# Performance work log

Measured on AMD Instinct MI355X. Metric: run time of the kernel, lower is better.

Reference implementation:

```python
import jax, jax.numpy as jnp
import numpy as np
from jax import lax

DIM = 2048
N_HEADS = 16
N_KV = 4
HEAD_DIM = DIM // N_HEADS  # 128
ROPE_BASE = 10000.0
SEQ = 4096
BSZ = 1


def bitlinear(x, W):
    # per-row abs-mean scale (detached), ternary round/clamp, straight-through blend
    s = lax.stop_gradient(jnp.clip(jnp.mean(jnp.abs(W), axis=1, keepdims=True), 1e-5, None))
    wt = jnp.clip(jnp.round(W / s), -1.0, 1.0)
    w = lax.stop_gradient(wt - W) + W  # straight-through
    return x @ (w * s).T


def rms_norm(x):
    eps = jnp.finfo(x.dtype).eps
    return x * lax.rsqrt(jnp.mean(x * x, axis=-1, keepdims=True) + eps)


def rope(x, cos, sin):
    half = x.shape[-1] // 2
    x1, x2 = x[..., :half], x[..., half:]
    return jnp.concatenate((x1 * cos + x2 * sin, -x1 * sin + x2 * cos), axis=-1)


def setup_inputs() -> dict:
    key = jax.random.key(0)
    ks = jax.random.split(key, 6)
    kv_dim = N_KV * HEAD_DIM
    return {
        "x": jax.random.normal(ks[0], (BSZ, SEQ, DIM), dtype=jnp.float32),
        "wq": jax.random.normal(ks[1], (DIM, DIM), dtype=jnp.float32) * 0.02,
        "wk": jax.random.normal(ks[2], (kv_dim, DIM), dtype=jnp.float32) * 0.02,
        "wv": jax.random.normal(ks[3], (kv_dim, DIM), dtype=jnp.float32) * 0.02,
        "wp": jax.random.normal(ks[4], (DIM, DIM), dtype=jnp.float32) * 0.02,
        "q_gain": jnp.ones((N_HEADS,), dtype=jnp.float32),
    }


def reference(x, wq, wk, wv, wp, q_gain):
    b, s, d = x.shape
    q = bitlinear(x, wq).reshape(b, s, N_HEADS, HEAD_DIM).transpose(0, 2, 1, 3)  # bhsd
    k = bitlinear(x, wk).reshape(b, s, N_KV, HEAD_DIM).transpose(0, 2, 1, 3)
    v = bitlinear(x, wv).reshape(b, s, N_KV, HEAD_DIM).transpose(0, 2, 1, 3)

    q = rms_norm(q)
    k = rms_norm(k)

    inv_freq = 1.0 / ROPE_BASE ** (jnp.arange(0, HEAD_DIM, 2, dtype=jnp.float32) / HEAD_DIM)
    t = jnp.arange(s, dtype=jnp.float32)
    freqs = jnp.outer(t, inv_freq)  # [s, hd/2]
    cos = jnp.cos(freqs)[None, None].astype(q.dtype)
    sin = jnp.sin(freqs)[None, None].astype(q.dtype)
    q = rope(q, cos, sin)
    k = rope(k, cos, sin)

    q = q * q_gain.astype(q.dtype)[None, :, None, None]

    groups = N_HEADS // N_KV
    k = jnp.repeat(k, groups, axis=1)  # GQA expand to [b, H, s, hd]
    v = jnp.repeat(v, groups, axis=1)

    scale = 1.0 / np.sqrt(HEAD_DIM)
    scores = jnp.einsum("bhqd,bhkd->bhqk", q, k) * scale
    causal = jnp.tril(jnp.ones((s, s), dtype=bool))
    scores = jnp.where(causal[None, None], scores, jnp.finfo(scores.dtype).min)
    attn = jax.nn.softmax(scores, axis=-1)
    y = jnp.einsum("bhqk,bhkd->bhqd", attn, v)

    y = y.transpose(0, 2, 1, 3).reshape(b, s, d)
    return bitlinear(y, wp)
```

## Files before the change

kernel.cpp:

```cpp
#include <hip/hip_runtime.h>
#include <math.h>

typedef unsigned short u16;
typedef short s16x8 __attribute__((ext_vector_type(8)));
typedef float f32x4 __attribute__((ext_vector_type(4)));
typedef u16 u16x4 __attribute__((ext_vector_type(4)));

static constexpr size_t OFF_XB   = 0;
static constexpr size_t OFF_WQKV = 16777216;
static constexpr size_t OFF_WP   = 29360128;
static constexpr size_t OFF_QKV  = 37748736;
static constexpr size_t OFF_PART = 37748736 + 16777216;
static constexpr size_t OFF_KH   = 88080384;
static constexpr size_t OFF_VT   = 92274688;

__device__ __forceinline__ u16 f2bf(float f) {
  union { float f; unsigned u; } v; v.f = f;
  unsigned r = v.u + 0x7fffu + ((v.u >> 16) & 1u);
  return (u16)(r >> 16);
}

__device__ __forceinline__ void async16(const u16* g, u16* lds) {
  __builtin_amdgcn_global_load_lds(
      (const __attribute__((address_space(1))) void*)g,
      (__attribute__((address_space(3))) void*)lds, 16, 0, 0);
}

__global__ __launch_bounds__(256) void quant_rows(const float* __restrict__ W,
                                                  u16* __restrict__ out) {
  const int row = blockIdx.x, tid = threadIdx.x;
  const float* src = W + (size_t)row * 2048 + tid * 8;
  float4 a = *(const float4*)(src);
  float4 b = *(const float4*)(src + 4);
  float asum = fabsf(a.x)+fabsf(a.y)+fabsf(a.z)+fabsf(a.w)
             + fabsf(b.x)+fabsf(b.y)+fabsf(b.z)+fabsf(b.w);
  #pragma unroll
  for (int off = 1; off < 64; off <<= 1) asum += __shfl_xor(asum, off, 64);
  __shared__ float red[4];
  if ((tid & 63) == 0) red[tid >> 6] = asum;
  __syncthreads();
  float s = fmaxf((red[0]+red[1]+red[2]+red[3]) * (1.0f/2048.0f), 1e-5f);
  float v[8] = {a.x,a.y,a.z,a.w,b.x,b.y,b.z,b.w};
  u16* dst = out + (size_t)row * 2048 + tid * 8;
  #pragma unroll
  for (int i = 0; i < 8; i++) {
    float q = rintf(v[i] / s);
    q = fminf(fmaxf(q, -1.f), 1.f);
    dst[i] = f2bf(q * s);
  }
}

__global__ __launch_bounds__(256) void cvt_bf16(const float* __restrict__ in,
                                                u16* __restrict__ out) {
  size_t i = ((size_t)blockIdx.x * 256 + threadIdx.x) * 4;
  float4 v = *(const float4*)(in + i);
  u16x4 o;
  o.x = f2bf(v.x); o.y = f2bf(v.y); o.z = f2bf(v.z); o.w = f2bf(v.w);
  *(u16x4*)(out + i) = o;
}

__global__ __launch_bounds__(256) void gemm_bt(const u16* __restrict__ A,
                                               const u16* __restrict__ B,
                                               float* __restrict__ C,
                                               int M, int N, int K) {
  __shared__ u16 sA[128 * 32];
  __shared__ u16 sB[128 * 32];
  const int tid = threadIdx.x;
  const int lane = tid & 63;
  const int wid = tid >> 6;
  const int lr = lane & 15, lq = lane >> 4;
  const int wm = (wid >> 1) * 64, wn = (wid & 1) * 64;
  const size_t m0 = (size_t)blockIdx.y * 128, n0 = (size_t)blockIdx.x * 128;

  const int r0 = tid >> 2, c0 = (tid & 3) * 8;
  const u16* Ab0 = A + (m0 + r0) * (size_t)K + c0;
  const u16* Ab1 = A + (m0 + 64 + r0) * (size_t)K + c0;
  const u16* Bb0 = B + (n0 + r0) * (size_t)K + c0;
  const u16* Bb1 = B + (n0 + 64 + r0) * (size_t)K + c0;
  u16* sA0 = &sA[tid * 8];
  u16* sA1 = &sA[(256 + tid) * 8];
  u16* sB0 = &sB[tid * 8];
  u16* sB1 = &sB[(256 + tid) * 8];

  f32x4 acc[4][4] = {};

  for (int kt = 0; kt < K; kt += 32) {
    async16(Ab0 + kt, sA0);
    async16(Ab1 + kt, sA1);
    async16(Bb0 + kt, sB0);
    async16(Bb1 + kt, sB1);
    __syncthreads();
    s16x8 af[4], bf[4];
    #pragma unroll
    for (int mt = 0; mt < 4; mt++)
      af[mt] = *(const s16x8*)&sA[(wm + mt * 16 + lr) * 32 + lq * 8];
    #pragma unroll
    for (int nt = 0; nt < 4; nt++)
      bf[nt] = *(const s16x8*)&sB[(wn + nt * 16 + lr) * 32 + lq * 8];
    #pragma unroll
    for (int mt = 0; mt < 4; mt++)
      #pragma unroll
      for (int nt = 0; nt < 4; nt++)
        acc[mt][nt] = __builtin_amdgcn_mfma_f32_16x16x32_bf16(af[mt], bf[nt], acc[mt][nt], 0, 0, 0);
    __syncthreads();
  }
  #pragma unroll
  for (int mt = 0; mt < 4; mt++)
    #pragma unroll
    for (int nt = 0; nt < 4; nt++)
      #pragma unroll
      for (int r = 0; r < 4; r++) {
        size_t m = m0 + wm + mt * 16 + lq * 4 + r;
        size_t n = n0 + wn + nt * 16 + lr;
        C[m * (size_t)N + n] = acc[mt][nt][r];
      }
}

__global__ __launch_bounds__(256) void prep_qk(const float* __restrict__ qkv,
                                               const float* __restrict__ qgain,
                                               u16* __restrict__ Qh,
                                               u16* __restrict__ Kh) {
  const int s = blockIdx.y;
  const int j = blockIdx.x * 4 + (threadIdx.x >> 6);
  const int t = threadIdx.x & 63;
  const float* row = qkv + (size_t)s * 3072 + (size_t)j * 128;
  float x1 = row[t], x2 = row[t + 64];
  float ss = x1 * x1 + x2 * x2;
  #pragma unroll
  for (int off = 1; off < 64; off <<= 1) ss += __shfl_xor(ss, off, 64);
  float rn = rsqrtf(ss * (1.0f / 128.0f) + 1.1920929e-07f);
  float invf = exp2f(-(float)t * 0.20762050593048096f);
  float ang = (float)s * invf;
  float sn, c;
  sincosf(ang, &sn, &c);
  if (j < 16) {
    float g = qgain[j] * 0.12751738f;
    float q1 = x1 * rn, q2 = x2 * rn;
    float o1 = (q1 * c + q2 * sn) * g;
    float o2 = (-q1 * sn + q2 * c) * g;
    u16* dst = Qh + ((size_t)j * 4096 + s) * 128;
    dst[t] = f2bf(o1); dst[t + 64] = f2bf(o2);
  } else {
    float k1 = x1 * rn, k2 = x2 * rn;
    float o1 = k1 * c + k2 * sn;
    float o2 = -k1 * sn + k2 * c;
    u16* dst = Kh + ((size_t)(j - 16) * 4096 + s) * 128;
    dst[t] = f2bf(o1); dst[t + 64] = f2bf(o2);
  }
}

__global__ __launch_bounds__(256) void vtrans(const float* __restrict__ qkv,
                                              u16* __restrict__ Vtg) {
  __shared__ float tile[64][67];
  const int tid = threadIdx.x;
  const int s0 = blockIdx.y * 64;
  const int c0 = blockIdx.x * 64;
  #pragma unroll
  for (int it = 0; it < 4; it++) {
    int i = it * 256 + tid;
    int r = i >> 4, c = (i & 15) * 4;
    float4 v = *(const float4*)(qkv + (size_t)(s0 + r) * 3072 + 2560 + c0 + c);
    tile[r][c] = v.x; tile[r][c + 1] = v.y; tile[r][c + 2] = v.z; tile[r][c + 3] = v.w;
  }
  __syncthreads();
  #pragma unroll
  for (int it = 0; it < 2; it++) {
    int i = it * 256 + tid;
    int dl = i >> 3, sc = (i & 7) * 8;
    s16x8 ov;
    #pragma unroll
    for (int jj = 0; jj < 8; jj++) ov[jj] = (short)f2bf(tile[sc + jj][dl]);
    *(s16x8*)&Vtg[(size_t)(c0 + dl) * 4096 + s0 + sc] = ov;
  }
}

__global__ __launch_bounds__(256, 2) void attn(const u16* __restrict__ Q,
                                               const u16* __restrict__ Kh,
                                               const u16* __restrict__ Vt,
                                               u16* __restrict__ Y,
                                               float* __restrict__ Opart,
                                               float* __restrict__ MLpart) {
  const int tid = threadIdx.x, lane = tid & 63, wid = tid >> 6;
  const int lr = lane & 15, lq = lane >> 4;

  int rem = blockIdx.x, s = 32;
  for (;;) {
    int cnt = (s >= 17 ? 32 : 0) + (((s & 1) == 0) ? 16 : 0);
    if (rem < cnt) break;
    rem -= cnt; --s;
  }
  int qt, chunk, h, split;
  if (s >= 17 && rem < 32) { split = 1; qt = s - 1; chunk = rem >> 4; h = rem & 15; }
  else { split = 0; if (s >= 17) rem -= 32; qt = (s >> 1) - 1; chunk = 0; h = rem & 15; }
  const int t0 = split ? chunk * (qt + 1) : 0;
  const int t1 = split ? t0 + qt + 1 : 2 * qt + 2;
  const int kvh = h >> 2;
  const int qbase = qt * 128;

  __shared__ u16 sK[64][136];
  __shared__ u16 sVt[144][72];
  __shared__ u16 sP[4][32][72];

  for (int i = tid; i < 16 * 72; i += 256) {
    int r = i / 72, c = i - r * 72;
    sVt[128 + r][c] = (r == 0) ? (u16)0x3F80 : (u16)0;
  }

  s16x8 qf[2][4];
  #pragma unroll
  for (int f = 0; f < 2; f++) {
    const u16* qp = Q + ((size_t)h * 4096 + qbase + wid * 32 + f * 16 + lr) * 128 + lq * 8;
    #pragma unroll
    for (int kc = 0; kc < 4; kc++) qf[f][kc] = *(const s16x8*)(qp + kc * 32);
  }

  f32x4 oacc[2][9] = {};
  float mrow[2][4];
  #pragma unroll
  for (int f = 0; f < 2; f++)
    #pragma unroll
    for (int r = 0; r < 4; r++) mrow[f][r] = -1e30f;

  const u16* Kbase = Kh + (size_t)kvh * 4096 * 128;
  const u16* Vbase = Vt + (size_t)kvh * 128 * 4096;

  for (int t = t0; t < t1; ++t) {
    #pragma unroll
    for (int it = 0; it < 4; it++) {
      int idx = it * 256 + tid;
      int kr = idx >> 4, kc8 = (idx & 15) * 8;
      *(s16x8*)&sK[kr][kc8] = *(const s16x8*)(Kbase + (size_t)(t * 64 + kr) * 128 + kc8);
    }
    #pragma unroll
    for (int it = 0; it < 4; it++) {
      int idx = it * 256 + tid;
      int vd = idx >> 3, vc = (idx & 7) * 8;
      *(s16x8*)&sVt[vd][vc] = *(const s16x8*)(Vbase + (size_t)vd * 4096 + t * 64 + vc);
    }
    __syncthreads();

    f32x4 sacc[2][4] = {};
    #pragma unroll
    for (int nt = 0; nt < 4; nt++)
      #pragma unroll
      for (int kc = 0; kc < 4; kc++) {
        s16x8 kf = *(const s16x8*)&sK[nt * 16 + lr][kc * 32 + lq * 8];
        sacc[0][nt] = __builtin_amdgcn_mfma_f32_16x16x32_bf16(qf[0][kc], kf, sacc[0][nt], 0, 0, 0);
        sacc[1][nt] = __builtin_amdgcn_mfma_f32_16x16x32_bf16(qf[1][kc], kf, sacc[1][nt], 0, 0, 0);
      }

    if (t >= 2 * qt) {
      #pragma unroll
      for (int f = 0; f < 2; f++) {
        int qr0 = qbase + wid * 32 + f * 16 + lq * 4;
        #pragma unroll
        for (int nt = 0; nt < 4; nt++) {
          int col = t * 64 + nt * 16 + lr;
          #pragma unroll
          for (int r = 0; r < 4; r++)
            if (col > qr0 + r) sacc[f][nt][r] = -1e30f;
        }
      }
    }

    float mx[2][4];
    #pragma unroll
    for (int f = 0; f < 2; f++)
      #pragma unroll
      for (int r = 0; r < 4; r++)
        mx[f][r] = fmaxf(fmaxf(sacc[f][0][r], sacc[f][1][r]),
                         fmaxf(sacc[f][2][r], sacc[f][3][r]));
    #pragma unroll
    for (int off = 1; off < 16; off <<= 1)
      #pragma unroll
      for (int f = 0; f < 2; f++)
        #pragma unroll
        for (int r = 0; r < 4; r++) mx[f][r] = fmaxf(mx[f][r], __shfl_xor(mx[f][r], off, 64));

    bool grow = false;
    #pragma unroll
    for (int f = 0; f < 2; f++)
      #pragma unroll
      for (int r = 0; r < 4; r++) grow = grow || (mx[f][r] > mrow[f][r]);
    if (__any(grow)) {
      float al[2][4];
      #pragma unroll
      for (int f = 0; f < 2; f++)
        #pragma unroll
        for (int r = 0; r < 4; r++) {
          float mn = fmaxf(mrow[f][r], mx[f][r]);
          al[f][r] = exp2f(mrow[f][r] - mn);
          mrow[f][r] = mn;
        }
      #pragma unroll
      for (int f = 0; f < 2; f++)
        #pragma unroll
        for (int dt = 0; dt < 9; dt++)
          #pragma unroll
          for (int r = 0; r < 4; r++) oacc[f][dt][r] *= al[f][r];
    }

    #pragma unroll
    for (int f = 0; f < 2; f++)
      #pragma unroll
      for (int nt = 0; nt < 4; nt++)
        #pragma unroll
        for (int r = 0; r < 4; r++) {
          union { float fv; unsigned u; } pu;
          pu.fv = exp2f(sacc[f][nt][r] - mrow[f][r]);
          sP[wid][f * 16 + lq * 4 + r][nt * 16 + lr] = (u16)(pu.u >> 16);
        }

    #pragma unroll
    for (int kc = 0; kc < 2; kc++) {
      s16x8 pf0 = *(const s16x8*)&sP[wid][lr][kc * 32 + lq * 8];
      s16x8 pf1 = *(const s16x8*)&sP[wid][16 + lr][kc * 32 + lq * 8];
      #pragma unroll
      for (int dt = 0; dt < 9; dt++) {
        s16x8 vf = *(const s16x8*)&sVt[dt * 16 + lr][kc * 32 + lq * 8];
        oacc[0][dt] = __builtin_amdgcn_mfma_f32_16x16x32_bf16(pf0, vf, oacc[0][dt], 0, 0, 0);
        oacc[1][dt] = __builtin_amdgcn_mfma_f32_16x16x32_bf16(pf1, vf, oacc[1][dt], 0, 0, 0);
      }
    }
    __syncthreads();
  }

  if (split) {
    const int pidx = ((qt - 16) * 16 + h) * 2 + chunk;
    float* Op = Opart + (size_t)pidx * 16384;
    #pragma unroll
    for (int f = 0; f < 2; f++)
      #pragma unroll
      for (int dt = 0; dt < 8; dt++)
        #pragma unroll
        for (int r = 0; r < 4; r++)
          Op[(wid * 32 + f * 16 + lq * 4 + r) * 128 + dt * 16 + lr] = oacc[f][dt][r];
    if (lr == 0) {
      #pragma unroll
      for (int f = 0; f < 2; f++)
        #pragma unroll
        for (int r = 0; r < 4; r++) {
          int row = wid * 32 + f * 16 + lq * 4 + r;
          MLpart[(size_t)pidx * 256 + row * 2]     = mrow[f][r];
          MLpart[(size_t)pidx * 256 + row * 2 + 1] = oacc[f][8][r];
        }
    }
  } else {
    #pragma unroll
    for (int f = 0; f < 2; f++) {
      float linv[4];
      #pragma unroll
      for (int r = 0; r < 4; r++) {
        float lv = __shfl(oacc[f][8][r], lane & 48);
        linv[r] = 1.0f / lv;
      }
      #pragma unroll
      for (int dt = 0; dt < 8; dt++)
        #pragma unroll
        for (int r = 0; r < 4; r++) {
          int q = qbase + wid * 32 + f * 16 + lq * 4 + r;
          Y[(size_t)q * 2048 + h * 128 + dt * 16 + lr] = f2bf(oacc[f][dt][r] * linv[r]);
        }
    }
  }
}

__global__ __launch_bounds__(256) void combine(const float* __restrict__ Op,
                                               const float* __restrict__ ML,
                                               u16* __restrict__ Y) {
  const int blk = blockIdx.x;
  const int qt16 = blk >> 4, h = blk & 15;
  const int p0 = blk * 2, p1 = p0 + 1;
  const int tid = threadIdx.x;
  const int row = tid >> 1, half = (tid & 1) * 64;
  float m0 = ML[(size_t)p0 * 256 + row * 2], l0 = ML[(size_t)p0 * 256 + row * 2 + 1];
  float m1 = ML[(size_t)p1 * 256 + row * 2], l1 = ML[(size_t)p1 * 256 + row * 2 + 1];
  float m = fmaxf(m0, m1);
  float w0 = exp2f(m0 - m), w1 = exp2f(m1 - m);
  float inv = 1.0f / (l0 * w0 + l1 * w1);
  w0 *= inv; w1 *= inv;
  const float* o0 = Op + (size_t)p0 * 16384 + row * 128 + half;
  const float* o1 = Op + (size_t)p1 * 16384 + row * 128 + half;
  size_t q = (size_t)(qt16 + 16) * 128 + row;
  u16* dst = Y + q * 2048 + h * 128 + half;
  #pragma unroll
  for (int c = 0; c < 64; c += 8) {
    float4 a0 = *(const float4*)(o0 + c), b0 = *(const float4*)(o0 + c + 4);
    float4 a1 = *(const float4*)(o1 + c), b1 = *(const float4*)(o1 + c + 4);
    u16 tmp[8];
    tmp[0] = f2bf(a0.x * w0 + a1.x * w1);
    tmp[1] = f2bf(a0.y * w0 + a1.y * w1);
    tmp[2] = f2bf(a0.z * w0 + a1.z * w1);
    tmp[3] = f2bf(a0.w * w0 + a1.w * w1);
    tmp[4] = f2bf(b0.x * w0 + b1.x * w1);
    tmp[5] = f2bf(b0.y * w0 + b1.y * w1);
    tmp[6] = f2bf(b0.z * w0 + b1.z * w1);
    tmp[7] = f2bf(b0.w * w0 + b1.w * w1);
    *(s16x8*)(dst + c) = *(s16x8*)tmp;
  }
}

extern "C" void kernel_launch(void* const* d_in, const int* in_sizes, int n_in,
                              void* d_out, int out_size, void* d_ws, size_t ws_size,
                              hipStream_t stream) {
  const float* x  = (const float*)d_in[0];
  const float* wq = (const float*)d_in[1];
  const float* wk = (const float*)d_in[2];
  const float* wv = (const float*)d_in[3];
  const float* wp = (const float*)d_in[4];
  const float* qg = (const float*)d_in[5];
  float* out = (float*)d_out;
  char* ws = (char*)d_ws;

  u16*   XB    = (u16*)(ws + OFF_XB);
  u16*   WQKV  = (u16*)(ws + OFF_WQKV);
  u16*   WP    = (u16*)(ws + OFF_WP);
  float* QKV   = (float*)(ws + OFF_QKV);
  u16*   QH    = XB;
  u16*   KH    = (u16*)(ws + OFF_KH);
  u16*   VT    = (u16*)(ws + OFF_VT);
  u16*   Yb    = (u16*)(ws + OFF_QKV);
  float* OPART = (float*)(ws + OFF_PART);
  float* MLP   = (float*)(ws + OFF_WQKV);

  quant_rows<<<2048, 256, 0, stream>>>(wq, WQKV);
  quant_rows<<<512,  256, 0, stream>>>(wk, WQKV + (size_t)2048 * 2048);
  quant_rows<<<512,  256, 0, stream>>>(wv, WQKV + (size_t)2560 * 2048);
  quant_rows<<<2048, 256, 0, stream>>>(wp, WP);
  cvt_bf16<<<8192, 256, 0, stream>>>(x, XB);
  gemm_bt<<<dim3(24, 32), 256, 0, stream>>>(XB, WQKV, QKV, 4096, 3072, 2048);
  prep_qk<<<dim3(5, 4096), 256, 0, stream>>>(QKV, qg, QH, KH);
  vtrans<<<dim3(8, 64), 256, 0, stream>>>(QKV, VT);
  attn<<<768, 256, 0, stream>>>(QH, KH, VT, Yb, OPART, MLP);
  combine<<<256, 256, 0, stream>>>(OPART, MLP, Yb);
  gemm_bt<<<dim3(16, 32), 256, 0, stream>>>(Yb, WP, out, 4096, 2048, 2048);
}
```

Measured before the change: 438.2 us.

## Compute transposed S so P stays in registers, drop LDS staging for P

Swaps the QK^T MFMA operands so each lane holds one query row across four keys, which lets the softmax probabilities feed the PV MFMA (16x16x16 variant) directly from registers instead of round-tripping through a shared-memory P buffer. The V tile is stored into LDS with a permuted column layout to match the new fragment order, row max reduction needs only two shuffles, and output stores become vectorized. It trades the LDS write/read of P and most cross-lane shuffles for twice as many smaller MFMA instructions and a more scattered V store pattern.

```diff
diff --git a/kernel.cpp b/kernel.cpp
--- a/kernel.cpp
+++ b/kernel.cpp
@@ -3,6 +3,7 @@
 
 typedef unsigned short u16;
 typedef short s16x8 __attribute__((ext_vector_type(8)));
+typedef short s16x4 __attribute__((ext_vector_type(4)));
 typedef float f32x4 __attribute__((ext_vector_type(4)));
 typedef u16 u16x4 __attribute__((ext_vector_type(4)));
 
@@ -199,7 +200,6 @@
 
   __shared__ u16 sK[64][136];
   __shared__ u16 sVt[144][72];
-  __shared__ u16 sP[4][32][72];
 
   for (int i = tid; i < 16 * 72; i += 256) {
     int r = i / 72, c = i - r * 72;
@@ -215,11 +215,7 @@
   }
 
   f32x4 oacc[2][9] = {};
-  float mrow[2][4];
-  #pragma unroll
-  for (int f = 0; f < 2; f++)
-    #pragma unroll
-    for (int r = 0; r < 4; r++) mrow[f][r] = -1e30f;
+  float mrow[2] = {-1e30f, -1e30f};
 
   const u16* Kbase = Kh + (size_t)kvh * 4096 * 128;
   const u16* Vbase = Vt + (size_t)kvh * 128 * 4096;
@@ -235,7 +231,13 @@
     for (int it = 0; it < 4; it++) {
       int idx = it * 256 + tid;
       int vd = idx >> 3, vc = (idx & 7) * 8;
-      *(s16x8*)&sVt[vd][vc] = *(const s16x8*)(Vbase + (size_t)vd * 4096 + t * 64 + vc);
+      s16x8 v = *(const s16x8*)(Vbase + (size_t)vd * 4096 + t * 64 + vc);
+      int g0 = ((vc >> 2) & 3) * 16 + (vc >> 4) * 4;
+      int g1 = ((((vc >> 2) & 3) + 1)) * 16 + (vc >> 4) * 4;
+      s16x4 lo = {v[0], v[1], v[2], v[3]};
+      s16x4 hi = {v[4], v[5], v[6], v[7]};
+      *(s16x4*)&sVt[vd][g0] = lo;
+      *(s16x4*)&sVt[vd][g1] = hi;
     }
     __syncthreads();
 
@@ -245,61 +247,51 @@
       #pragma unroll
       for (int kc = 0; kc < 4; kc++) {
         s16x8 kf = *(const s16x8*)&sK[nt * 16 + lr][kc * 32 + lq * 8];
-        sacc[0][nt] = __builtin_amdgcn_mfma_f32_16x16x32_bf16(qf[0][kc], kf, sacc[0][nt], 0, 0, 0);
-        sacc[1][nt] = __builtin_amdgcn_mfma_f32_16x16x32_bf16(qf[1][kc], kf, sacc[1][nt], 0, 0, 0);
+        sacc[0][nt] = __builtin_amdgcn_mfma_f32_16x16x32_bf16(kf, qf[0][kc], sacc[0][nt], 0, 0, 0);
+        sacc[1][nt] = __builtin_amdgcn_mfma_f32_16x16x32_bf16(kf, qf[1][kc], sacc[1][nt], 0, 0, 0);
       }
 
     if (t >= 2 * qt) {
       #pragma unroll
       for (int f = 0; f < 2; f++) {
-        int qr0 = qbase + wid * 32 + f * 16 + lq * 4;
+        int qg = qbase + wid * 32 + f * 16 + lr;
         #pragma unroll
         for (int nt = 0; nt < 4; nt++) {
-          int col = t * 64 + nt * 16 + lr;
+          int kv0 = t * 64 + nt * 16 + lq * 4;
           #pragma unroll
           for (int r = 0; r < 4; r++)
-            if (col > qr0 + r) sacc[f][nt][r] = -1e30f;
+            if (kv0 + r > qg) sacc[f][nt][r] = -1e30f;
         }
       }
     }
 
-    float mx[2][4];
-    #pragma unroll
-    for (int f = 0; f < 2; f++)
-      #pragma unroll
-      for (int r = 0; r < 4; r++)
-        mx[f][r] = fmaxf(fmaxf(sacc[f][0][r], sacc[f][1][r]),
-                         fmaxf(sacc[f][2][r], sacc[f][3][r]));
-    #pragma unroll
-    for (int off = 1; off < 16; off <<= 1)
-      #pragma unroll
-      for (int f = 0; f < 2; f++)
-        #pragma unroll
-        for (int r = 0; r < 4; r++) mx[f][r] = fmaxf(mx[f][r], __shfl_xor(mx[f][r], off, 64));
-
-    bool grow = false;
-    #pragma unroll
-    for (int f = 0; f < 2; f++)
-      #pragma unroll
-      for (int r = 0; r < 4; r++) grow = grow || (mx[f][r] > mrow[f][r]);
+    float mx[2];
+    #pragma unroll
+    for (int f = 0; f < 2; f++) {
+      float m01 = fmaxf(fmaxf(sacc[f][0][0], sacc[f][0][1]), fmaxf(sacc[f][0][2], sacc[f][0][3]));
+      float m23 = fmaxf(fmaxf(sacc[f][1][0], sacc[f][1][1]), fmaxf(sacc[f][1][2], sacc[f][1][3]));
+      float m45 = fmaxf(fmaxf(sacc[f][2][0], sacc[f][2][1]), fmaxf(sacc[f][2][2], sacc[f][2][3]));
+      float m67 = fmaxf(fmaxf(sacc[f][3][0], sacc[f][3][1]), fmaxf(sacc[f][3][2], sacc[f][3][3]));
+      mx[f] = fmaxf(fmaxf(m01, m23), fmaxf(m45, m67));
+      mx[f] = fmaxf(mx[f], __shfl_xor(mx[f], 16, 64));
+      mx[f] = fmaxf(mx[f], __shfl_xor(mx[f], 32, 64));
+    }
+
+    bool grow = (mx[0] > mrow[0]) || (mx[1] > mrow[1]);
     if (__any(grow)) {
-      float al[2][4];
-      #pragma unroll
-      for (int f = 0; f < 2; f++)
-        #pragma unroll
-        for (int r = 0; r < 4; r++) {
-          float mn = fmaxf(mrow[f][r], mx[f][r]);
-          al[f][r] = exp2f(mrow[f][r] - mn);
-          mrow[f][r] = mn;
-        }
-      #pragma unroll
-      for (int f = 0; f < 2; f++)
+      #pragma unroll
+      for (int f = 0; f < 2; f++) {
+        float mn = fmaxf(mrow[f], mx[f]);
+        float al = exp2f(mrow[f] - mn);
+        mrow[f] = mn;
         #pragma unroll
         for (int dt = 0; dt < 9; dt++)
           #pragma unroll
-          for (int r = 0; r < 4; r++) oacc[f][dt][r] *= al[f][r];
-    }
-
+          for (int r = 0; r < 4; r++) oacc[f][dt][r] *= al;
+      }
+    }
+
+    s16x4 pf[2][4];
     #pragma unroll
     for (int f = 0; f < 2; f++)
       #pragma unroll
@@ -307,19 +299,24 @@
         #pragma unroll
         for (int r = 0; r < 4; r++) {
           union { float fv; unsigned u; } pu;
-          pu.fv = exp2f(sacc[f][nt][r] - mrow[f][r]);
-          sP[wid][f * 16 + lq * 4 + r][nt * 16 + lr] = (u16)(pu.u >> 16);
+          pu.fv = exp2f(sacc[f][nt][r] - mrow[f]);
+          pf[f][nt][r] = (short)(pu.u >> 16);
         }
 
     #pragma unroll
-    for (int kc = 0; kc < 2; kc++) {
-      s16x8 pf0 = *(const s16x8*)&sP[wid][lr][kc * 32 + lq * 8];
-      s16x8 pf1 = *(const s16x8*)&sP[wid][16 + lr][kc * 32 + lq * 8];
-      #pragma unroll
-      for (int dt = 0; dt < 9; dt++) {
-        s16x8 vf = *(const s16x8*)&sVt[dt * 16 + lr][kc * 32 + lq * 8];
-        oacc[0][dt] = __builtin_amdgcn_mfma_f32_16x16x32_bf16(pf0, vf, oacc[0][dt], 0, 0, 0);
-        oacc[1][dt] = __builtin_amdgcn_mfma_f32_16x16x32_bf16(pf1, vf, oacc[1][dt], 0, 0, 0);
+    for (int dt = 0; dt < 9; dt++) {
+      s16x8 v01 = *(const s16x8*)&sVt[dt * 16 + lr][lq * 16];
+      s16x8 v23 = *(const s16x8*)&sVt[dt * 16 + lr][lq * 16 + 8];
+      s16x4 vf0 = {v01[0], v01[1], v01[2], v01[3]};
+      s16x4 vf1 = {v01[4], v01[5], v01[6], v01[7]};
+      s16x4 vf2 = {v23[0], v23[1], v23[2], v23[3]};
+      s16x4 vf3 = {v23[4], v23[5], v23[6], v23[7]};
+      #pragma unroll
+      for (int f = 0; f < 2; f++) {
+        oacc[f][dt] = __builtin_amdgcn_mfma_f32_16x16x16bf16_1k(vf0, pf[f][0], oacc[f][dt], 0, 0, 0);
+        oacc[f][dt] = __builtin_amdgcn_mfma_f32_16x16x16bf16_1k(vf1, pf[f][1], oacc[f][dt], 0, 0, 0);
+        oacc[f][dt] = __builtin_amdgcn_mfma_f32_16x16x16bf16_1k(vf2, pf[f][2], oacc[f][dt], 0, 0, 0);
+        oacc[f][dt] = __builtin_amdgcn_mfma_f32_16x16x16bf16_1k(vf3, pf[f][3], oacc[f][dt], 0, 0, 0);
       }
     }
     __syncthreads();
@@ -329,38 +326,33 @@
     const int pidx = ((qt - 16) * 16 + h) * 2 + chunk;
     float* Op = Opart + (size_t)pidx * 16384;
     #pragma unroll
-    for (int f = 0; f < 2; f++)
+    for (int f = 0; f < 2; f++) {
+      int row = wid * 32 + f * 16 + lr;
       #pragma unroll
       for (int dt = 0; dt < 8; dt++)
+        *(f32x4*)&Op[row * 128 + dt * 16 + lq * 4] = oacc[f][dt];
+    }
+    if (lq == 0) {
+      #pragma unroll
+      for (int f = 0; f < 2; f++) {
+        int row = wid * 32 + f * 16 + lr;
+        MLpart[(size_t)pidx * 256 + row * 2]     = mrow[f];
+        MLpart[(size_t)pidx * 256 + row * 2 + 1] = oacc[f][8][0];
+      }
+    }
+  } else {
+    #pragma unroll
+    for (int f = 0; f < 2; f++) {
+      float lv = __shfl(oacc[f][8][0], lr, 64);
+      float linv = 1.0f / lv;
+      int qg = qbase + wid * 32 + f * 16 + lr;
+      #pragma unroll
+      for (int dt = 0; dt < 8; dt++) {
+        u16 tmp[4];
         #pragma unroll
-        for (int r = 0; r < 4; r++)
-          Op[(wid * 32 + f * 16 + lq * 4 + r) * 128 + dt * 16 + lr] = oacc[f][dt][r];
-    if (lr == 0) {
-      #pragma unroll
-      for (int f = 0; f < 2; f++)
-        #pragma unroll
-        for (int r = 0; r < 4; r++) {
-          int row = wid * 32 + f * 16 + lq * 4 + r;
-          MLpart[(size_t)pidx * 256 + row * 2]     = mrow[f][r];
-          MLpart[(size_t)pidx * 256 + row * 2 + 1] = oacc[f][8][r];
-        }
-    }
-  } else {
-    #pragma unroll
-    for (int f = 0; f < 2; f++) {
-      float linv[4];
-      #pragma unroll
-      for (int r = 0; r < 4; r++) {
-        float lv = __shfl(oacc[f][8][r], lane & 48);
-        linv[r] = 1.0f / lv;
-      }
-      #pragma unroll
-      for (int dt = 0; dt < 8; dt++)
-        #pragma unroll
-        for (int r = 0; r < 4; r++) {
-          int q = qbase + wid * 32 + f * 16 + lq * 4 + r;
-          Y[(size_t)q * 2048 + h * 128 + dt * 16 + lr] = f2bf(oacc[f][dt][r] * linv[r]);
-        }
+        for (int r = 0; r < 4; r++) tmp[r] = f2bf(oacc[f][dt][r] * linv);
+        *(s16x4*)&Y[(size_t)qg * 2048 + h * 128 + dt * 16 + lq * 4] = *(s16x4*)tmp;
+      }
     }
   }
 }
```

Result: no change. 430.2 us (-1.8%).
